# Kernel optimization log

Hardware: AMD Instinct MI355X
Metric: run time of the kernel (lower is better)

The kernel has to match this reference:

```python
import jax, jax.numpy as jnp
import numpy as np

EPS = 1e-3  # keras BatchNormalization default epsilon


def _ngf(atoms, bonds, edges, W, b):
    """NeuralGraphHidden: neighbor gather + per-degree dense.
    atoms [B,N,Fa], bonds [B,N,D,Fb], edges [B,N,D] (-1 padded),
    W [D+1, Fa+Fb, width], b [D+1, width] -> [B,N,width]."""
    B, N, Fa = atoms.shape
    D = edges.shape[-1]
    deg = jnp.sum(edges != -1, axis=-1)  # [B,N] atom degrees
    # zero-row padded lookup table so edge index -1 gathers zeros
    apad = jnp.concatenate([jnp.zeros((B, 1, Fa), atoms.dtype), atoms], axis=1)
    neigh = jax.vmap(lambda a, e: a[e])(apad, edges + 1)  # [B,N,D,Fa]
    summed_atom = atoms + neigh.sum(axis=2)  # include_self=True
    summed_bond = bonds.sum(axis=2)
    feats = jnp.concatenate([summed_atom, summed_bond], axis=-1)  # [B,N,Fa+Fb]
    # dense transform for every degree, then select by actual degree
    all_out = jnp.einsum('bnf,dfw->bdnw', feats, W) + b[None, :, None, :]
    mask = (deg[:, None, :] == jnp.arange(D + 1)[None, :, None]).astype(atoms.dtype)
    return jnp.einsum('bdnw,bdn->bnw', all_out, mask)


def _bn(x, g, beta, m, v):
    return g * (x - m) * jax.lax.rsqrt(v + EPS) + beta


def setup_inputs() -> dict:
    key = jax.random.key(0)
    ks = jax.random.split(key, 32)
    B, N, D, Fa, Fb = 1024, 60, 5, 62, 6
    widths = [128, 128, 128]
    KSZ, FILT = 16, 128

    atoms = jax.random.normal(ks[0], (B, N, Fa), jnp.float32)
    bonds = jax.random.uniform(ks[1], (B, N, D, Fb), dtype=jnp.float32)
    edges = jax.random.randint(ks[2], (B, N, D), -1, N).astype(jnp.int32)

    def glorot(k, shape):
        s = jnp.sqrt(2.0 / (shape[-2] + shape[-1])).astype(jnp.float32)
        return jax.random.normal(k, shape, jnp.float32) * s

    inp = dict(atoms=atoms, bonds=bonds, edges=edges)
    fins = [Fa + Fb, widths[0] + Fb, widths[1] + Fb]
    for i in range(3):
        inp['W%d' % (i + 1)] = glorot(ks[3 + i], (D + 1, fins[i], widths[i]))
        inp['b%d' % (i + 1)] = 0.01 * jax.random.normal(ks[6 + i], (D + 1, widths[i]), jnp.float32)
    inp['Wc'] = glorot(ks[9], (KSZ, widths[2], FILT))
    for i, c in enumerate([widths[0], widths[1], widths[2], FILT]):
        inp['bn%d_g' % (i + 1)] = 1.0 + 0.1 * jax.random.normal(ks[10 + i], (c,), jnp.float32)
        inp['bn%d_b' % (i + 1)] = 0.1 * jax.random.normal(ks[14 + i], (c,), jnp.float32)
        inp['bn%d_m' % (i + 1)] = 0.1 * jax.random.normal(ks[18 + i], (c,), jnp.float32)
        inp['bn%d_v' % (i + 1)] = jax.random.uniform(ks[22 + i], (c,), jnp.float32, 0.5, 1.5)
    return inp


def reference(atoms, bonds, edges, W1, b1, W2, b2, W3, b3, Wc,
              bn1_g, bn1_b, bn1_m, bn1_v, bn2_g, bn2_b, bn2_m, bn2_v,
              bn3_g, bn3_b, bn3_m, bn3_v, bn4_g, bn4_b, bn4_m, bn4_v):
    x = jax.nn.relu(_bn(_ngf(atoms, bonds, edges, W1, b1), bn1_g, bn1_b, bn1_m, bn1_v))
    x = jax.nn.relu(_bn(_ngf(x, bonds, edges, W2, b2), bn2_g, bn2_b, bn2_m, bn2_v))
    x = jax.nn.relu(_bn(_ngf(x, bonds, edges, W3, b3), bn3_g, bn3_b, bn3_m, bn3_v))
    # Conv1D over the atom axis, VALID padding, no bias
    x = jax.lax.conv_general_dilated(x, Wc, window_strides=(1,), padding='VALID',
                                     dimension_numbers=('NWC', 'WIO', 'NWC'))
    x = jax.nn.relu(_bn(x, bn4_g, bn4_b, bn4_m, bn4_v))
    # dropout is identity at inference
    return x
```

## Files before the change

kernel.cpp:

```cpp
#include <hip/hip_runtime.h>
#include <hip/hip_bf16.h>

typedef __attribute__((ext_vector_type(8))) short bf16x8;
typedef __attribute__((ext_vector_type(4))) short short4v;
typedef __attribute__((ext_vector_type(4))) float f32x4;
typedef unsigned short u16;
typedef unsigned char u8;

static constexpr size_t OFF_BN   = 0;
static constexpr size_t OFF_SH2  = 4096;
static constexpr size_t OFF_BSUM = 13312;
static constexpr size_t OFF_WT1  = 750592;
static constexpr size_t OFF_WT2  = 898048;
static constexpr size_t OFF_WT3  = 1143808;
static constexpr size_t OFF_WCF  = 1389568;

__device__ __forceinline__ float bf2f(u16 r) {
  union { unsigned u; float f; } cv; cv.u = ((unsigned)r) << 16; return cv.f;
}
__device__ __forceinline__ u16 f2bf(float x) {
  __hip_bfloat16 h = __float2bfloat16(x); return *(u16*)&h;
}
__device__ __forceinline__ int xts(int c, int n) {
  return c * 64 + (((n >> 3) ^ (c & 7)) << 3) + (n & 7);
}

__device__ __forceinline__ void emit_wt(u16* dst, const float* W, int FIN, int FIN_A,
                                        int CB, int KSTEPS, int v) {
  int lane = v & 63;
  int ftile = (v >> 6) & 7;
  int ks = (v >> 9) % KSTEPS;
  int d = (v >> 9) / KSTEPS;
  int f = ftile * 16 + (lane & 15);
  int k0 = ks * 32 + (lane >> 4) * 8;
  bf16x8 o;
  #pragma unroll
  for (int i = 0; i < 8; ++i) {
    int k = k0 + i;
    int src = (k < FIN_A) ? k : (k >= CB && k < CB + 6) ? (FIN_A + k - CB) : -1;
    float x = (src >= 0) ? W[((size_t)d * FIN + src) * 128 + f] : 0.f;
    o[i] = (short)f2bf(x);
  }
  *reinterpret_cast<bf16x8*>(&dst[(size_t)v * 8]) = o;
}

__global__ __launch_bounds__(256) void prep(
    const float* __restrict__ bonds, const float* __restrict__ Wc,
    const float* __restrict__ W1, const float* __restrict__ W2, const float* __restrict__ W3,
    const float* g1, const float* be1, const float* m1, const float* v1,
    const float* g2, const float* be2, const float* m2, const float* v2,
    const float* g3, const float* be3, const float* m3, const float* v3,
    const float* g4, const float* be4, const float* m4, const float* v4,
    const float* bb1, const float* bb2, const float* bb3,
    float* __restrict__ scale, float* __restrict__ shift, float* __restrict__ shift2,
    u16* __restrict__ bsum, u16* __restrict__ wt1, u16* __restrict__ wt2,
    u16* __restrict__ wt3, u16* __restrict__ wcf) {
  __shared__ float sb[3840];
  const int b = blockIdx.x, tid = threadIdx.x;
  if (b < 480) {
    const int base = b * 128;
    const float4* src = (const float4*)(bonds + (size_t)base * 30);
    for (int i = tid; i < 960; i += 256) ((float4*)sb)[i] = src[i];
    __syncthreads();
    if (tid < 128) {
      float s[6] = {0.f, 0.f, 0.f, 0.f, 0.f, 0.f};
      #pragma unroll
      for (int d = 0; d < 5; ++d)
        #pragma unroll
        for (int j = 0; j < 6; ++j) s[j] += sb[tid * 30 + d * 6 + j];
      #pragma unroll
      for (int j = 0; j < 6; ++j) bsum[(size_t)(base + tid) * 6 + j] = f2bf(s[j]);
    }
  } else if (b < 608) {
    int v = (b - 480) * 256 + tid;
    int lane = v & 63, ftile = (v >> 6) & 7, ks = v >> 9;
    int f = ftile * 16 + (lane & 15);
    int k0 = ks * 32 + (lane >> 4) * 8;
    int tap = k0 >> 7, ch0 = k0 & 127;
    bf16x8 o;
    #pragma unroll
    for (int i = 0; i < 8; ++i)
      o[i] = (short)f2bf(Wc[((size_t)tap * 128 + ch0 + i) * 128 + f]);
    *reinterpret_cast<bf16x8*>(&wcf[(size_t)v * 8]) = o;
  } else if (b < 644) {
    emit_wt(wt1, W1, 68, 62, 64, 3, (b - 608) * 256 + tid);
  } else if (b < 704) {
    emit_wt(wt2, W2, 134, 128, 128, 5, (b - 644) * 256 + tid);
  } else if (b < 764) {
    emit_wt(wt3, W3, 134, 128, 128, 5, (b - 704) * 256 + tid);
  } else if (b < 766) {
    int idx = (b - 764) * 256 + tid;
    const float* gs[4] = {g1, g2, g3, g4};
    const float* bs[4] = {be1, be2, be3, be4};
    const float* ms[4] = {m1, m2, m3, m4};
    const float* vs[4] = {v1, v2, v3, v4};
    int l = idx >> 7, ch = idx & 127;
    float sc = gs[l][ch] / sqrtf(vs[l][ch] + 1e-3f);
    scale[idx] = sc;
    shift[idx] = bs[l][ch] - ms[l][ch] * sc;
  } else {
    int i = (b - 766) * 256 + tid;
    if (i < 2304) {
      const float* G[3] = {g1, g2, g3};
      const float* Be[3] = {be1, be2, be3};
      const float* M[3] = {m1, m2, m3};
      const float* V[3] = {v1, v2, v3};
      const float* Bl[3] = {bb1, bb2, bb3};
      int ll = i / 768, r = i % 768, f = r & 127;
      float sc = G[ll][f] / sqrtf(V[ll][f] + 1e-3f);
      float sh = Be[ll][f] - M[ll][f] * sc;
      shift2[i] = Bl[ll][r] * sc + sh;
    }
  }
}

template <int MPW, int CB, int KSTEPS, bool TOCONV>
__device__ __forceinline__ void layer(
    u16* __restrict__ feats, u16* __restrict__ xbt,
    const u8* __restrict__ S8, const u8* __restrict__ degs8,
    const int* __restrict__ presentS, const u16* __restrict__ bsum_b,
    const u16* __restrict__ wtf, const float* __restrict__ sc_l,
    const float* __restrict__ sh2_l, int tid, int lane, int wid) {
  const int fr = lane & 15, rg = lane >> 4;

  bf16x8 sf[4][2];
  #pragma unroll
  for (int nt = 0; nt < 4; ++nt) {
    #pragma unroll
    for (int ks = 0; ks < 2; ++ks) {
      int n = nt * 16 + fr, m0 = ks * 32 + rg * 8;
      const unsigned* wp = (const unsigned*)(S8 + n * 64 + m0);
      unsigned lo = wp[0], hi = wp[1];
      bf16x8 v;
      #pragma unroll
      for (int i = 0; i < 4; ++i) v[i] = (short)f2bf((float)((lo >> (i * 8)) & 255u));
      #pragma unroll
      for (int i = 0; i < 4; ++i) v[4 + i] = (short)f2bf((float)((hi >> (i * 8)) & 255u));
      sf[nt][ks] = v;
    }
  }

  f32x4 gacc[MPW][4];
  #pragma unroll
  for (int mt = 0; mt < MPW; ++mt)
    #pragma unroll
    for (int nt = 0; nt < 4; ++nt) gacc[mt][nt] = (f32x4){0.f, 0.f, 0.f, 0.f};
  #pragma unroll
  for (int mt = 0; mt < MPW; ++mt) {
    const int c = (wid * MPW + mt) * 16 + fr;
    #pragma unroll
    for (int ks = 0; ks < 2; ++ks) {
      const int m0 = ks * 32 + rg * 8;
      bf16x8 a = *reinterpret_cast<const bf16x8*>(
          &xbt[c * 64 + (((m0 >> 3) ^ (c & 7)) << 3)]);
      #pragma unroll
      for (int nt = 0; nt < 4; ++nt)
        gacc[mt][nt] = __builtin_amdgcn_mfma_f32_16x16x32_bf16(a, sf[nt][ks],
                                                               gacc[mt][nt], 0, 0, 0);
    }
  }
  #pragma unroll
  for (int mt = 0; mt < MPW; ++mt) {
    const int c0 = (wid * MPW + mt) * 16 + rg * 4;
    const int uu = c0 >> 3;
    #pragma unroll
    for (int nt = 0; nt < 4; ++nt) {
      const int n = nt * 16 + fr;
      if (n < 60) {
        short4v p;
        #pragma unroll
        for (int j = 0; j < 4; ++j) p[j] = (short)f2bf(gacc[mt][nt][j]);
        *reinterpret_cast<short4v*>(
            &feats[n * 160 + ((uu ^ (n & 7)) << 3) + (c0 & 7)]) = p;
      }
    }
  }
  for (int i = tid; i < 360; i += 256) {
    int n = i / 6, c = CB + (i % 6);
    int u = c >> 3;
    int uu2 = (u < 16) ? (u ^ (n & 7)) : u;
    feats[n * 160 + (uu2 << 3) + (c & 7)] = bsum_b[i];
  }
  __syncthreads();

  const int pres = *presentS;
  int dg[4];
  #pragma unroll
  for (int nt = 0; nt < 4; ++nt) dg[nt] = degs8[nt * 16 + fr];
  float4 scv[2];
  #pragma unroll
  for (int mt = 0; mt < 2; ++mt)
    scv[mt] = *reinterpret_cast<const float4*>(&sc_l[(wid * 2 + mt) * 16 + rg * 4]);

  for (int d = 0; d < 6; ++d) {
    if (!(pres & (1 << d))) continue;
    f32x4 acc[2][4];
    #pragma unroll
    for (int mt = 0; mt < 2; ++mt)
      #pragma unroll
      for (int nt = 0; nt < 4; ++nt) acc[mt][nt] = (f32x4){0.f, 0.f, 0.f, 0.f};
    const u16* __restrict__ wd = wtf + (size_t)d * KSTEPS * 4096;
    bf16x8 acur[2], anxt[2];
    #pragma unroll
    for (int mt = 0; mt < 2; ++mt)
      acur[mt] = *reinterpret_cast<const bf16x8*>(
          &wd[((0 * 8 + wid * 2 + mt) * 64 + lane) * 8]);
    #pragma unroll
    for (int ks = 0; ks < KSTEPS; ++ks) {
      if (ks + 1 < KSTEPS) {
        #pragma unroll
        for (int mt = 0; mt < 2; ++mt)
          anxt[mt] = *reinterpret_cast<const bf16x8*>(
              &wd[(((ks + 1) * 8 + wid * 2 + mt) * 64 + lane) * 8]);
      }
      bf16x8 bfr[4];
      const int u = (ks * 32 + rg * 8) >> 3;
      #pragma unroll
      for (int nt = 0; nt < 4; ++nt) {
        const int n = nt * 16 + fr;
        const int uu2 = (u < 16) ? (u ^ (n & 7)) : u;
        bfr[nt] = *reinterpret_cast<const bf16x8*>(&feats[n * 160 + (uu2 << 3)]);
      }
      #pragma unroll
      for (int mt = 0; mt < 2; ++mt)
        #pragma unroll
        for (int nt = 0; nt < 4; ++nt)
          acc[mt][nt] = __builtin_amdgcn_mfma_f32_16x16x32_bf16(acur[mt], bfr[nt],
                                                                acc[mt][nt], 0, 0, 0);
      #pragma unroll
      for (int mt = 0; mt < 2; ++mt) acur[mt] = anxt[mt];
    }
    #pragma unroll
    for (int mt = 0; mt < 2; ++mt) {
      const int f0 = (wid * 2 + mt) * 16 + rg * 4;
      float4 shv = *reinterpret_cast<const float4*>(&sh2_l[d * 128 + f0]);
      #pragma unroll
      for (int nt = 0; nt < 4; ++nt) {
        const int n = nt * 16 + fr;
        if (n < 60 && dg[nt] == d) {
          float y0 = fmaxf(acc[mt][nt][0] * scv[mt].x + shv.x, 0.f);
          float y1 = fmaxf(acc[mt][nt][1] * scv[mt].y + shv.y, 0.f);
          float y2 = fmaxf(acc[mt][nt][2] * scv[mt].z + shv.z, 0.f);
          float y3 = fmaxf(acc[mt][nt][3] * scv[mt].w + shv.w, 0.f);
          if (TOCONV) {
            short4v p = {(short)f2bf(y0), (short)f2bf(y1),
                         (short)f2bf(y2), (short)f2bf(y3)};
            *reinterpret_cast<short4v*>(
                &xbt[n * 128 + (((f0 >> 3) ^ (n & 7)) << 3) + (f0 & 7)]) = p;
          } else {
            xbt[xts(f0 + 0, n)] = f2bf(y0);
            xbt[xts(f0 + 1, n)] = f2bf(y1);
            xbt[xts(f0 + 2, n)] = f2bf(y2);
            xbt[xts(f0 + 3, n)] = f2bf(y3);
          }
        }
      }
    }
  }
  __syncthreads();
}

__global__ __launch_bounds__(256, 4) void mega(
    const float* __restrict__ atoms, const int* __restrict__ edges_g,
    const u16* __restrict__ bsum, const u16* __restrict__ wt1,
    const u16* __restrict__ wt2, const u16* __restrict__ wt3,
    const u16* __restrict__ wcf, const float* __restrict__ scale,
    const float* __restrict__ shift, const float* __restrict__ shift2,
    float* __restrict__ out) {
  __shared__ __align__(16) char smem[39808];
  u16* feats = (u16*)smem;
  u16* xbt = (u16*)(smem + 19200);
  u8* S8 = (u8*)(smem + 35584);
  signed char* eds = (signed char*)(smem + 39424);
  u8* degs8 = (u8*)(smem + 39728);
  int* presentS = (int*)(smem + 39792);

  const int b = blockIdx.x, tid = threadIdx.x;
  const int lane = tid & 63;
  const int wid = __builtin_amdgcn_readfirstlane(tid >> 6);

  if (tid == 0) *presentS = 0;
  for (int i = tid; i < 1200; i += 256) ((int4*)feats)[i] = (int4){0, 0, 0, 0};
  for (int i = tid; i < 240; i += 256) ((int4*)S8)[i] = (int4){0, 0, 0, 0};
  for (int i = tid; i < 300; i += 256) eds[i] = (signed char)edges_g[b * 300 + i];
  for (int i = tid; i < 8192; i += 256) {
    int n = i >> 7, c = i & 127;
    float x = (c < 62 && n < 60) ? atoms[(size_t)b * 3720 + n * 62 + c] : 0.f;
    xbt[xts(c, n)] = f2bf(x);
  }
  __syncthreads();

  if (tid < 64) {
    int dgv = 7;
    if (tid < 60) {
      dgv = 0;
      #pragma unroll
      for (int d = 0; d < 5; ++d) dgv += (eds[tid * 5 + d] >= 0);
      atomicOr(presentS, 1 << dgv);
      S8[tid * 64 + tid] = (u8)(S8[tid * 64 + tid] + 1);
      #pragma unroll
      for (int d = 0; d < 5; ++d) {
        int e = eds[tid * 5 + d];
        if (e >= 0) S8[tid * 64 + e] = (u8)(S8[tid * 64 + e] + 1);
      }
    }
    degs8[tid] = (u8)dgv;
  }
  __syncthreads();

  const u16* bsum_b = bsum + (size_t)b * 360;
  layer<1, 64, 3, false>(feats, xbt, S8, degs8, presentS, bsum_b, wt1,
                         scale + 0, shift2 + 0, tid, lane, wid);
  layer<2, 128, 5, false>(feats, xbt, S8, degs8, presentS, bsum_b, wt2,
                          scale + 128, shift2 + 768, tid, lane, wid);
  layer<2, 128, 5, true>(feats, xbt, S8, degs8, presentS, bsum_b, wt3,
                         scale + 256, shift2 + 1536, tid, lane, wid);

  {
    const int fr = lane & 15, rg = lane >> 4;
    const u16* xconv = xbt;
    f32x4 cacc[3][2];
    #pragma unroll
    for (int rt = 0; rt < 3; ++rt)
      #pragma unroll
      for (int ct = 0; ct < 2; ++ct) cacc[rt][ct] = (f32x4){0.f, 0.f, 0.f, 0.f};

    bf16x8 br[2][2], ar[2][3];
    auto loadB = [&](int ks, int slot) {
      #pragma unroll
      for (int nt = 0; nt < 2; ++nt)
        br[slot][nt] = *reinterpret_cast<const bf16x8*>(
            &wcf[(((size_t)ks * 8 + wid * 2 + nt) * 64 + lane) * 8]);
    };
    auto loadA = [&](int ks, int slot) {
      int rowadd = ks >> 2;
      int unit = ((ks & 3) << 2) + rg;
      #pragma unroll
      for (int rt = 0; rt < 3; ++rt) {
        int arow = rt * 16 + fr + rowadd;
        int uo = unit ^ (arow & 7);
        ar[slot][rt] = *reinterpret_cast<const bf16x8*>(&xconv[arow * 128 + uo * 8]);
      }
    };
    loadB(0, 0); loadB(1, 1); loadA(0, 0);
    #pragma unroll 2
    for (int ks = 0; ks < 64; ++ks) {
      if (ks < 63) loadA(ks + 1, (ks + 1) & 1);
      #pragma unroll
      for (int rt = 0; rt < 3; ++rt)
        #pragma unroll
        for (int ct = 0; ct < 2; ++ct)
          cacc[rt][ct] = __builtin_amdgcn_mfma_f32_16x16x32_bf16(
              ar[ks & 1][rt], br[ks & 1][ct], cacc[rt][ct], 0, 0, 0);
      if (ks < 62) loadB(ks + 2, ks & 1);
    }

    #pragma unroll
    for (int ct = 0; ct < 2; ++ct) {
      int f = wid * 32 + ct * 16 + fr;
      float sc = scale[384 + f], sh = shift[384 + f];
      #pragma unroll
      for (int rt = 0; rt < 3; ++rt) {
        #pragma unroll
        for (int j = 0; j < 4; ++j) {
          int t = rt * 16 + rg * 4 + j;
          if (t < 45) {
            float y = fmaxf(cacc[rt][ct][j] * sc + sh, 0.f);
            out[((size_t)b * 45 + t) * 128 + f] = y;
          }
        }
      }
    }
  }
}

extern "C" void kernel_launch(void* const* d_in, const int* in_sizes, int n_in,
                              void* d_out, int out_size, void* d_ws, size_t ws_size,
                              hipStream_t stream) {
  const float* atoms = (const float*)d_in[0];
  const float* bonds = (const float*)d_in[1];
  const int*   edges = (const int*)d_in[2];
  const float* W1 = (const float*)d_in[3]; const float* b1 = (const float*)d_in[4];
  const float* W2 = (const float*)d_in[5]; const float* b2 = (const float*)d_in[6];
  const float* W3 = (const float*)d_in[7]; const float* b3 = (const float*)d_in[8];
  const float* Wc = (const float*)d_in[9];

  char* ws = (char*)d_ws;
  float* scale  = (float*)(ws + OFF_BN);
  float* shift  = scale + 512;
  float* shift2 = (float*)(ws + OFF_SH2);
  u16*   bsum   = (u16*)(ws + OFF_BSUM);
  u16*   wt1    = (u16*)(ws + OFF_WT1);
  u16*   wt2    = (u16*)(ws + OFF_WT2);
  u16*   wt3    = (u16*)(ws + OFF_WT3);
  u16*   wcf    = (u16*)(ws + OFF_WCF);

  prep<<<775, 256, 0, stream>>>(
      bonds, Wc, W1, W2, W3,
      (const float*)d_in[10], (const float*)d_in[11], (const float*)d_in[12], (const float*)d_in[13],
      (const float*)d_in[14], (const float*)d_in[15], (const float*)d_in[16], (const float*)d_in[17],
      (const float*)d_in[18], (const float*)d_in[19], (const float*)d_in[20], (const float*)d_in[21],
      (const float*)d_in[22], (const float*)d_in[23], (const float*)d_in[24], (const float*)d_in[25],
      b1, b2, b3, scale, shift, shift2, bsum, wt1, wt2, wt3, wcf);

  mega<<<1024, 256, 0, stream>>>(atoms, edges, bsum, wt1, wt2, wt3, wcf,
                                 scale, shift, shift2, (float*)d_out);
}
```

Before: 215.9 us.

## Restructure layer epilogues with register select, swapped MFMA operands, deeper weight prefetch

For the non-conv layers, the MFMA operands are swapped so that atoms form the A side and weights the B side. Per-degree results are then merged in registers with a select, and a single vectorized transposed store is written at the end instead of scattered per-element stores inside the degree loop. The weight loads use a two-deep ring prefetch, and the conv loop B prefetch is deepened from two to three stages with unroll 4. Atom loading now stages coalesced float4 global reads into shared scratch before transposing into bf16x8 vectors, and only the needed regions are zeroed instead of whole buffers. This adds register pressure and extra select ALU work per degree.

```diff
diff --git a/kernel.cpp b/kernel.cpp
--- a/kernel.cpp
+++ b/kernel.cpp
@@ -21,8 +21,10 @@
 __device__ __forceinline__ u16 f2bf(float x) {
   __hip_bfloat16 h = __float2bfloat16(x); return *(u16*)&h;
 }
-__device__ __forceinline__ int xts(int c, int n) {
-  return c * 64 + (((n >> 3) ^ (c & 7)) << 3) + (n & 7);
+__device__ __forceinline__ int fidx(int n, int c) {
+  int u = c >> 3;
+  int uu = (u < 16) ? (u ^ (n & 7)) : u;
+  return n * 160 + (uu << 3) + (c & 7);
 }
 
 __device__ __forceinline__ void emit_wt(u16* dst, const float* W, int FIN, int FIN_A,
@@ -177,82 +179,175 @@
   }
   for (int i = tid; i < 360; i += 256) {
     int n = i / 6, c = CB + (i % 6);
-    int u = c >> 3;
-    int uu2 = (u < 16) ? (u ^ (n & 7)) : u;
-    feats[n * 160 + (uu2 << 3) + (c & 7)] = bsum_b[i];
+    feats[fidx(n, c)] = bsum_b[i];
   }
   __syncthreads();
 
   const int pres = *presentS;
-  int dg[4];
-  #pragma unroll
-  for (int nt = 0; nt < 4; ++nt) dg[nt] = degs8[nt * 16 + fr];
-  float4 scv[2];
-  #pragma unroll
-  for (int mt = 0; mt < 2; ++mt)
-    scv[mt] = *reinterpret_cast<const float4*>(&sc_l[(wid * 2 + mt) * 16 + rg * 4]);
-
-  for (int d = 0; d < 6; ++d) {
-    if (!(pres & (1 << d))) continue;
-    f32x4 acc[2][4];
+
+  if constexpr (!TOCONV) {
+    const int f0w = wid * 32;
+    unsigned dgw[4];
+    #pragma unroll
+    for (int m = 0; m < 4; ++m)
+      dgw[m] = *(const unsigned*)(degs8 + m * 16 + rg * 4);
+    float scf[2] = {sc_l[f0w + fr], sc_l[f0w + 16 + fr]};
+    f32x4 racc[4][2];
+    #pragma unroll
+    for (int m = 0; m < 4; ++m)
+      #pragma unroll
+      for (int nf = 0; nf < 2; ++nf) racc[m][nf] = (f32x4){0.f, 0.f, 0.f, 0.f};
+
+    for (int d = 0; d < 6; ++d) {
+      if (!(pres & (1 << d))) continue;
+      const u16* __restrict__ wd = wtf + (size_t)d * (KSTEPS * 4096);
+      f32x4 acc[4][2];
+      #pragma unroll
+      for (int m = 0; m < 4; ++m)
+        #pragma unroll
+        for (int nf = 0; nf < 2; ++nf) acc[m][nf] = (f32x4){0.f, 0.f, 0.f, 0.f};
+      bf16x8 wring[2][2];
+      #pragma unroll
+      for (int nf = 0; nf < 2; ++nf)
+        wring[0][nf] = *reinterpret_cast<const bf16x8*>(
+            &wd[((0 * 8 + wid * 2 + nf) * 64 + lane) * 8]);
+      #pragma unroll
+      for (int nf = 0; nf < 2; ++nf)
+        wring[1][nf] = *reinterpret_cast<const bf16x8*>(
+            &wd[((1 * 8 + wid * 2 + nf) * 64 + lane) * 8]);
+      #pragma unroll
+      for (int ks = 0; ks < KSTEPS; ++ks) {
+        bf16x8 afr[4];
+        const int u = ks * 4 + rg;
+        #pragma unroll
+        for (int m = 0; m < 4; ++m) {
+          const int n = m * 16 + fr;
+          const int uu = (u < 16) ? (u ^ (n & 7)) : u;
+          afr[m] = *reinterpret_cast<const bf16x8*>(&feats[n * 160 + (uu << 3)]);
+        }
+        #pragma unroll
+        for (int m = 0; m < 4; ++m)
+          #pragma unroll
+          for (int nf = 0; nf < 2; ++nf)
+            acc[m][nf] = __builtin_amdgcn_mfma_f32_16x16x32_bf16(
+                afr[m], wring[ks & 1][nf], acc[m][nf], 0, 0, 0);
+        if (ks + 2 < KSTEPS) {
+          #pragma unroll
+          for (int nf = 0; nf < 2; ++nf)
+            wring[ks & 1][nf] = *reinterpret_cast<const bf16x8*>(
+                &wd[(((ks + 2) * 8 + wid * 2 + nf) * 64 + lane) * 8]);
+        }
+      }
+      #pragma unroll
+      for (int nf = 0; nf < 2; ++nf) {
+        const float sh = sh2_l[d * 128 + f0w + nf * 16 + fr];
+        #pragma unroll
+        for (int m = 0; m < 4; ++m) {
+          #pragma unroll
+          for (int j = 0; j < 4; ++j) {
+            float y = fmaxf(acc[m][nf][j] * scf[nf] + sh, 0.f);
+            bool sel = (((dgw[m] >> (8 * j)) & 255u) == (unsigned)d);
+            racc[m][nf][j] = sel ? y : racc[m][nf][j];
+          }
+        }
+      }
+    }
+    #pragma unroll
+    for (int m = 0; m < 4; ++m) {
+      const int n0 = m * 16 + rg * 4;
+      if (n0 < 60) {
+        #pragma unroll
+        for (int nf = 0; nf < 2; ++nf) {
+          const int c = f0w + nf * 16 + fr;
+          short4v p;
+          #pragma unroll
+          for (int j = 0; j < 4; ++j) p[j] = (short)f2bf(racc[m][nf][j]);
+          *reinterpret_cast<short4v*>(
+              &xbt[c * 64 + (((n0 >> 3) ^ (c & 7)) << 3) + (n0 & 7)]) = p;
+        }
+      }
+    }
+  } else {
+    int dgn[4];
+    #pragma unroll
+    for (int nt = 0; nt < 4; ++nt) dgn[nt] = degs8[nt * 16 + fr];
+    f32x4 scv[2];
     #pragma unroll
     for (int mt = 0; mt < 2; ++mt)
-      #pragma unroll
-      for (int nt = 0; nt < 4; ++nt) acc[mt][nt] = (f32x4){0.f, 0.f, 0.f, 0.f};
-    const u16* __restrict__ wd = wtf + (size_t)d * KSTEPS * 4096;
-    bf16x8 acur[2], anxt[2];
+      scv[mt] = *reinterpret_cast<const f32x4*>(&sc_l[(wid * 2 + mt) * 16 + rg * 4]);
+    f32x4 racc[2][4];
     #pragma unroll
     for (int mt = 0; mt < 2; ++mt)
-      acur[mt] = *reinterpret_cast<const bf16x8*>(
-          &wd[((0 * 8 + wid * 2 + mt) * 64 + lane) * 8]);
-    #pragma unroll
-    for (int ks = 0; ks < KSTEPS; ++ks) {
-      if (ks + 1 < KSTEPS) {
+      #pragma unroll
+      for (int nt = 0; nt < 4; ++nt) racc[mt][nt] = (f32x4){0.f, 0.f, 0.f, 0.f};
+
+    for (int d = 0; d < 6; ++d) {
+      if (!(pres & (1 << d))) continue;
+      const u16* __restrict__ wd = wtf + (size_t)d * (KSTEPS * 4096);
+      f32x4 acc[2][4];
+      #pragma unroll
+      for (int mt = 0; mt < 2; ++mt)
+        #pragma unroll
+        for (int nt = 0; nt < 4; ++nt) acc[mt][nt] = (f32x4){0.f, 0.f, 0.f, 0.f};
+      bf16x8 wring[2][2];
+      #pragma unroll
+      for (int mt = 0; mt < 2; ++mt)
+        wring[0][mt] = *reinterpret_cast<const bf16x8*>(
+            &wd[((0 * 8 + wid * 2 + mt) * 64 + lane) * 8]);
+      #pragma unroll
+      for (int mt = 0; mt < 2; ++mt)
+        wring[1][mt] = *reinterpret_cast<const bf16x8*>(
+            &wd[((1 * 8 + wid * 2 + mt) * 64 + lane) * 8]);
+      #pragma unroll
+      for (int ks = 0; ks < KSTEPS; ++ks) {
+        bf16x8 bfr[4];
+        const int u = ks * 4 + rg;
+        #pragma unroll
+        for (int nt = 0; nt < 4; ++nt) {
+          const int n = nt * 16 + fr;
+          const int uu = (u < 16) ? (u ^ (n & 7)) : u;
+          bfr[nt] = *reinterpret_cast<const bf16x8*>(&feats[n * 160 + (uu << 3)]);
+        }
         #pragma unroll
         for (int mt = 0; mt < 2; ++mt)
-          anxt[mt] = *reinterpret_cast<const bf16x8*>(
-              &wd[(((ks + 1) * 8 + wid * 2 + mt) * 64 + lane) * 8]);
-      }
-      bf16x8 bfr[4];
-      const int u = (ks * 32 + rg * 8) >> 3;
-      #pragma unroll
-      for (int nt = 0; nt < 4; ++nt) {
-        const int n = nt * 16 + fr;
-        const int uu2 = (u < 16) ? (u ^ (n & 7)) : u;
-        bfr[nt] = *reinterpret_cast<const bf16x8*>(&feats[n * 160 + (uu2 << 3)]);
-      }
-      #pragma unroll
-      for (int mt = 0; mt < 2; ++mt)
-        #pragma unroll
-        for (int nt = 0; nt < 4; ++nt)
-          acc[mt][nt] = __builtin_amdgcn_mfma_f32_16x16x32_bf16(acur[mt], bfr[nt],
-                                                                acc[mt][nt], 0, 0, 0);
-      #pragma unroll
-      for (int mt = 0; mt < 2; ++mt) acur[mt] = anxt[mt];
-    }
-    #pragma unroll
-    for (int mt = 0; mt < 2; ++mt) {
-      const int f0 = (wid * 2 + mt) * 16 + rg * 4;
-      float4 shv = *reinterpret_cast<const float4*>(&sh2_l[d * 128 + f0]);
-      #pragma unroll
-      for (int nt = 0; nt < 4; ++nt) {
-        const int n = nt * 16 + fr;
-        if (n < 60 && dg[nt] == d) {
-          float y0 = fmaxf(acc[mt][nt][0] * scv[mt].x + shv.x, 0.f);
-          float y1 = fmaxf(acc[mt][nt][1] * scv[mt].y + shv.y, 0.f);
-          float y2 = fmaxf(acc[mt][nt][2] * scv[mt].z + shv.z, 0.f);
-          float y3 = fmaxf(acc[mt][nt][3] * scv[mt].w + shv.w, 0.f);
-          if (TOCONV) {
-            short4v p = {(short)f2bf(y0), (short)f2bf(y1),
-                         (short)f2bf(y2), (short)f2bf(y3)};
-            *reinterpret_cast<short4v*>(
-                &xbt[n * 128 + (((f0 >> 3) ^ (n & 7)) << 3) + (f0 & 7)]) = p;
-          } else {
-            xbt[xts(f0 + 0, n)] = f2bf(y0);
-            xbt[xts(f0 + 1, n)] = f2bf(y1);
-            xbt[xts(f0 + 2, n)] = f2bf(y2);
-            xbt[xts(f0 + 3, n)] = f2bf(y3);
+          #pragma unroll
+          for (int nt = 0; nt < 4; ++nt)
+            acc[mt][nt] = __builtin_amdgcn_mfma_f32_16x16x32_bf16(
+                wring[ks & 1][mt], bfr[nt], acc[mt][nt], 0, 0, 0);
+        if (ks + 2 < KSTEPS) {
+          #pragma unroll
+          for (int mt = 0; mt < 2; ++mt)
+            wring[ks & 1][mt] = *reinterpret_cast<const bf16x8*>(
+                &wd[(((ks + 2) * 8 + wid * 2 + mt) * 64 + lane) * 8]);
+        }
+      }
+      #pragma unroll
+      for (int mt = 0; mt < 2; ++mt) {
+        f32x4 shv = *reinterpret_cast<const f32x4*>(
+            &sh2_l[d * 128 + (wid * 2 + mt) * 16 + rg * 4]);
+        #pragma unroll
+        for (int nt = 0; nt < 4; ++nt) {
+          bool sel = (dgn[nt] == d);
+          #pragma unroll
+          for (int j = 0; j < 4; ++j) {
+            float y = fmaxf(acc[mt][nt][j] * scv[mt][j] + shv[j], 0.f);
+            racc[mt][nt][j] = sel ? y : racc[mt][nt][j];
           }
+        }
+      }
+    }
+    #pragma unroll
+    for (int nt = 0; nt < 4; ++nt) {
+      const int n = nt * 16 + fr;
+      if (n < 60) {
+        #pragma unroll
+        for (int mt = 0; mt < 2; ++mt) {
+          const int f0 = (wid * 2 + mt) * 16 + rg * 4;
+          short4v p;
+          #pragma unroll
+          for (int j = 0; j < 4; ++j) p[j] = (short)f2bf(racc[mt][nt][j]);
+          *reinterpret_cast<short4v*>(
+              &xbt[n * 128 + (((f0 >> 3) ^ (n & 7)) << 3) + (f0 & 7)]) = p;
         }
       }
     }
@@ -267,26 +362,30 @@
     const u16* __restrict__ wcf, const float* __restrict__ scale,
     const float* __restrict__ shift, const float* __restrict__ shift2,
     float* __restrict__ out) {
-  __shared__ __align__(16) char smem[39808];
+  __shared__ __align__(16) char smem[39936];
   u16* feats = (u16*)smem;
   u16* xbt = (u16*)(smem + 19200);
   u8* S8 = (u8*)(smem + 35584);
   signed char* eds = (signed char*)(smem + 39424);
   u8* degs8 = (u8*)(smem + 39728);
   int* presentS = (int*)(smem + 39792);
+  float* fscr = (float*)smem;
 
   const int b = blockIdx.x, tid = threadIdx.x;
   const int lane = tid & 63;
   const int wid = __builtin_amdgcn_readfirstlane(tid >> 6);
 
   if (tid == 0) *presentS = 0;
-  for (int i = tid; i < 1200; i += 256) ((int4*)feats)[i] = (int4){0, 0, 0, 0};
-  for (int i = tid; i < 240; i += 256) ((int4*)S8)[i] = (int4){0, 0, 0, 0};
   for (int i = tid; i < 300; i += 256) eds[i] = (signed char)edges_g[b * 300 + i];
-  for (int i = tid; i < 8192; i += 256) {
-    int n = i >> 7, c = i & 127;
-    float x = (c < 62 && n < 60) ? atoms[(size_t)b * 3720 + n * 62 + c] : 0.f;
-    xbt[xts(c, n)] = f2bf(x);
+  {
+    const float4* ag4 = (const float4*)(atoms + (size_t)b * 3720);
+    float4* fs4 = (float4*)fscr;
+    for (int i = tid; i < 930; i += 256) fs4[i] = ag4[i];
+    int4 z4 = {0, 0, 0, 0};
+    int4* xz = (int4*)(xbt + 64 * 64);
+    for (int i = tid; i < 512; i += 256) xz[i] = z4;
+    int4* sz = (int4*)S8;
+    for (int i = tid; i < 240; i += 256) sz[i] = z4;
   }
   __syncthreads();
 
@@ -306,7 +405,24 @@
     }
     degs8[tid] = (u8)dgv;
   }
+  for (int id = tid; id < 512; id += 256) {
+    int oct = id & 7, c = id >> 3;
+    bf16x8 v;
+    #pragma unroll
+    for (int k = 0; k < 8; ++k) {
+      int n = oct * 8 + k;
+      float x = (c < 62 && n < 60) ? fscr[n * 62 + c] : 0.f;
+      v[k] = (short)f2bf(x);
+    }
+    *reinterpret_cast<bf16x8*>(&xbt[c * 64 + ((oct ^ (c & 7)) << 3)]) = v;
+  }
   __syncthreads();
+
+  for (int i = tid; i < 60 * 52; i += 256) {
+    int n = i / 52, q = i % 52;
+    int c = (q < 26) ? (70 + q) : (108 + q);
+    feats[fidx(n, c)] = 0;
+  }
 
   const u16* bsum_b = bsum + (size_t)b * 360;
   layer<1, 64, 3, false>(feats, xbt, S8, degs8, presentS, bsum_b, wt1,
@@ -325,7 +441,7 @@
       #pragma unroll
       for (int ct = 0; ct < 2; ++ct) cacc[rt][ct] = (f32x4){0.f, 0.f, 0.f, 0.f};
 
-    bf16x8 br[2][2], ar[2][3];
+    bf16x8 br[4][2], ar[2][3];
     auto loadB = [&](int ks, int slot) {
       #pragma unroll
       for (int nt = 0; nt < 2; ++nt)
@@ -342,8 +458,8 @@
         ar[slot][rt] = *reinterpret_cast<const bf16x8*>(&xconv[arow * 128 + uo * 8]);
       }
     };
-    loadB(0, 0); loadB(1, 1); loadA(0, 0);
-    #pragma unroll 2
+    loadB(0, 0); loadB(1, 1); loadB(2, 2); loadA(0, 0);
+    #pragma unroll 4
     for (int ks = 0; ks < 64; ++ks) {
       if (ks < 63) loadA(ks + 1, (ks + 1) & 1);
       #pragma unroll
@@ -351,8 +467,8 @@
         #pragma unroll
         for (int ct = 0; ct < 2; ++ct)
           cacc[rt][ct] = __builtin_amdgcn_mfma_f32_16x16x32_bf16(
-              ar[ks & 1][rt], br[ks & 1][ct], cacc[rt][ct], 0, 0, 0);
-      if (ks < 62) loadB(ks + 2, ks & 1);
+              ar[ks & 1][rt], br[ks & 3][ct], cacc[rt][ct], 0, 0, 0);
+      if (ks < 61) loadB(ks + 3, (ks + 3) & 3);
     }
 
     #pragma unroll
```

Measured after the change: 202.9 us. -6.0%, faster.
